# Kernel tuning notes

Hardware: AMD Instinct MI355X
Metric: run time of the kernel (lower is better)

## Reference

```python
import jax, jax.numpy as jnp
import numpy as np

GROUPS = 2
EPS = 1e-5


def channel_shuffle(x, groups=2):
    b, c, h, w = x.shape
    x = x.reshape(b, groups, c // groups, h, w)
    x = jnp.transpose(x, (0, 2, 1, 3, 4))
    return x.reshape(b, c, h, w)


def binarize_weight(w):
    # w: (O, I/g, k, k). scaling_factor = mean |w| over (in,kh,kw), detached.
    scale = jax.lax.stop_gradient(jnp.mean(jnp.abs(w), axis=(1, 2, 3), keepdims=True))
    bw = scale * jnp.sign(w)
    cl = jnp.clip(w, -1.0, 1.0)
    # STE: forward value = bw, gradient flows through clamp
    return jax.lax.stop_gradient(bw) - jax.lax.stop_gradient(cl) + cl


@jax.custom_vjp
def bin_act(x):
    return jnp.sign(x)


def _bin_act_fwd(x):
    return jnp.sign(x), x


def _bin_act_bwd(x, g):
    scale = jnp.where((x >= 1.0) | (x <= -1.0), 0.01, 1.0)
    return (g * scale,)


bin_act.defvjp(_bin_act_fwd, _bin_act_bwd)


def grouped_bin_conv(x, w, pad):
    return jax.lax.conv_general_dilated(
        x, binarize_weight(w), window_strides=(1, 1),
        padding=[(pad, pad), (pad, pad)],
        dimension_numbers=('NCHW', 'OIHW', 'NCHW'),
        feature_group_count=GROUPS)


def batchnorm(x, gamma, beta):
    # training-mode BN: biased batch statistics over (N,H,W)
    mu = jnp.mean(x, axis=(0, 2, 3), keepdims=True)
    var = jnp.mean((x - mu) ** 2, axis=(0, 2, 3), keepdims=True)
    xn = (x - mu) * jax.lax.rsqrt(var + EPS)
    return xn * gamma[None, :, None, None] + beta[None, :, None, None]


def add_bias(x, b):
    return x + b[None, :, None, None]


def prelu(x, a):
    return jnp.where(x >= 0, x, a[None, :, None, None] * x)


def setup_inputs() -> dict:
    key = jax.random.key(0)
    ks = jax.random.split(key, 4)
    C, half = 256, 128
    x = jax.random.normal(ks[0], (32, C, 56, 56), dtype=jnp.float32)
    # two BinaryConvs (64,128,3,3) stacked -> grouped (128,128,3,3)
    w3 = jax.random.uniform(ks[1], (half, C // GROUPS, 3, 3), dtype=jnp.float32) * 0.001
    w1 = jax.random.uniform(ks[2], (half, C // GROUPS, 1, 1), dtype=jnp.float32) * 0.001
    z = jnp.zeros((C,), jnp.float32)
    return {
        'x': x, 'w3': w3, 'w1': w1,
        'b1': z, 'g1': jnp.ones((half,), jnp.float32), 'be1': jnp.zeros((half,), jnp.float32),
        'b2_1': z, 'a2': jnp.full((C,), 0.25, jnp.float32), 'b2_2': z,
        'b3_1': z, 'g3': jnp.ones((half,), jnp.float32), 'be3': jnp.zeros((half,), jnp.float32),
        'b4_1': z, 'a4': jnp.full((C,), 0.25, jnp.float32), 'b4_2': z,
    }


def reference(x, w3, w1, b1, g1, be1, b2_1, a2, b2_2, b3_1, g3, be3, b4_1, a4, b4_2):
    half = w3.shape[0]  # out_channel // 2 = 128
    x = channel_shuffle(x, GROUPS)
    x1 = bin_act(add_bias(x, b1))
    x1 = batchnorm(grouped_bin_conv(x1, w3, pad=1), g1, be1)
    x1_res = x[:, half:]
    x1 = x1 + x[:, :half]
    x2 = jnp.concatenate([x1, x1_res], axis=1)
    x2 = add_bias(prelu(add_bias(x2, b2_1), a2), b2_2)
    x2 = add_bias(x2, b3_1)
    x3 = bin_act(x2)
    x3 = batchnorm(grouped_bin_conv(x3, w1, pad=0), g3, be3)
    x3_res = x2[:, half:]
    x3 = x3 + x2[:, :half]
    x4 = jnp.concatenate([x3, x3_res], axis=1)
    x5 = add_bias(prelu(add_bias(x4, b4_1), a4), b4_2)
    return x5
```

## Files before the change

### kernel.cpp

```cpp
#include <hip/hip_runtime.h>
#include <stdint.h>

typedef unsigned short ushort_t;
typedef unsigned int uint_t;
typedef _Float16 half_t;

typedef float  float4_t __attribute__((ext_vector_type(4)));
typedef float  float2_t __attribute__((ext_vector_type(2)));
typedef _Float16 half4_t __attribute__((ext_vector_type(4)));
typedef _Float16 half2_t __attribute__((ext_vector_type(2)));
typedef uint_t uint4_t  __attribute__((ext_vector_type(4)));
typedef uint_t uint2_t  __attribute__((ext_vector_type(2)));

#define B_N 32
#define C_N 256
#define HALF_N 128
#define H_N 56
#define W_N 56
#define HW_N 3136
#define NPIX (B_N * HW_N)
#define EPS_D 1e-5
#define W3S 40
#define PWS 16

__global__ void prep_kernel(const float* __restrict__ w3, const float* __restrict__ w1,
                            uint_t* __restrict__ wbits3, uint_t* __restrict__ wbits1,
                            uint_t* __restrict__ popcw3,
                            double* __restrict__ scale3, double* __restrict__ scale1,
                            double* __restrict__ sums1, double* __restrict__ sums2,
                            uint_t* __restrict__ oflags) {
    __shared__ double red[128];
    __shared__ int ipw[2][9];
    __shared__ int flsh[2];
    int t = threadIdx.x;
    int blk = blockIdx.x;
    int lane = t & 63;
    int wv = t >> 6;
    if (blk == 0) {
        sums1[t] = 0.0; sums1[128 + t] = 0.0;
        sums2[t] = 0.0; sums2[128 + t] = 0.0;
    }
    if (blk < 128) {
        int o = blk;
        double acc = 0.0;
        int anynp = 0;
        #pragma unroll
        for (int j = 0; j < 9; ++j) {
            float v = w3[o * 1152 + t * 9 + j];
            acc += fabs((double)v);
            anynp |= (v <= 0.f) ? 1 : 0;
            unsigned long long b = __ballot(v > 0.f);
            if (lane == 0) {
                wbits3[o * W3S + j * 4 + wv * 2 + 0] = (uint_t)b;
                wbits3[o * W3S + j * 4 + wv * 2 + 1] = (uint_t)(b >> 32);
                ipw[wv][j] = __popcll(b);
            }
        }
        unsigned long long m = __ballot(anynp != 0);
        if (lane == 0) flsh[wv] = (m != 0ull) ? 1 : 0;
        red[t] = acc; __syncthreads();
        for (int s = 64; s > 0; s >>= 1) { if (t < s) red[t] += red[t + s]; __syncthreads(); }
        if (t == 0) { scale3[o] = red[0] / 1152.0; oflags[o] = (uint_t)(flsh[0] | flsh[1]); }
        if (t < 9) popcw3[o * PWS + t] = (uint_t)(ipw[0][t] + ipw[1][t]);
    } else {
        int o = blk - 128;
        float v = w1[o * 128 + t];
        unsigned long long b = __ballot(v > 0.f);
        unsigned long long m = __ballot(v <= 0.f);
        if (lane == 0) {
            wbits1[o * 8 + wv * 2 + 0] = (uint_t)b;
            wbits1[o * 8 + wv * 2 + 1] = (uint_t)(b >> 32);
            flsh[wv] = (m != 0ull) ? 1 : 0;
        }
        red[t] = fabs((double)v); __syncthreads();
        for (int s = 64; s > 0; s >>= 1) { if (t < s) red[t] += red[t + s]; __syncthreads(); }
        if (t == 0) { scale1[o] = red[0] / 128.0; oflags[128 + o] = (uint_t)(flsh[0] | flsh[1]); }
    }
}

__global__ __launch_bounds__(256) void sign1_kernel(const float* __restrict__ x,
                                                    const float* __restrict__ b1,
                                                    uint_t* __restrict__ vb,
                                                    const uint_t* __restrict__ oflags,
                                                    uint_t* __restrict__ fin) {
    __shared__ int fl[4];
    int t = threadIdx.x;
    if (blockIdx.x == 0 && blockIdx.y == 0) {
        int lane = t & 63, wv4 = t >> 6;
        uint_t f = oflags[t];
        unsigned long long m = __ballot(f != 0u);
        if (lane == 0) fl[wv4] = (m != 0ull) ? 1 : 0;
        __syncthreads();
        if (t == 0) { fin[0] = (uint_t)(fl[0] | fl[1]); fin[1] = (uint_t)(fl[2] | fl[3]); }
    }
    int p = blockIdx.x * 512 + t * 2;
    int cb = blockIdx.y * 32;
    int b = p / HW_N;
    int hw = p - b * HW_N;
    const float* xb = x + (size_t)b * C_N * HW_N + hw;
    uint_t w0 = 0, w1 = 0;
    #pragma unroll
    for (int j = 0; j < 32; ++j) {
        int c = cb + j;
        int src = ((c & 1) << 7) + (c >> 1);
        float2_t xv = *(const float2_t*)(xb + (size_t)src * HW_N);
        double bc = (double)b1[c];
        if ((double)xv[0] + bc > 0.0) w0 |= (1u << j);
        if ((double)xv[1] + bc > 0.0) w1 |= (1u << j);
    }
    uint2_t o2; o2[0] = w0; o2[1] = w1;
    *(uint2_t*)(vb + (size_t)(cb >> 5) * NPIX + p) = o2;
}

__global__ __launch_bounds__(256) void conv3_kernel(const uint_t* __restrict__ vb,
                                                    const uint_t* __restrict__ wbits3,
                                                    const uint_t* __restrict__ popcw3,
                                                    half_t* __restrict__ yh,
                                                    double* __restrict__ sums,
                                                    const uint_t* __restrict__ fin) {
    __shared__ short dlds[32][258];
    __shared__ int partS[8][32];
    __shared__ int partS2[8][32];
    int t = threadIdx.x;
    int lane = t & 63;
    int wv = t >> 6;
    bool fast = (fin[0] == 0u);
    int yb = blockIdx.y;
    if (fast && (yb & 1)) return;
    int g = yb >> 1;
    int oh = yb & 1;
    int o0 = g * 64 + oh * 32;
    int p = blockIdx.x * 256 + t;
    int hw = p % HW_N;
    int h = hw / W_N;
    int w = hw - h * W_N;
    const uint_t* vbase = vb + (size_t)g * 4 * NPIX;

    uint_t v[9][4];
    int inv[9];
    int nvalid = 0;
    #pragma unroll
    for (int j = 0; j < 9; ++j) {
        int kh = j / 3 - 1, kw = j - (j / 3) * 3 - 1;
        int hh = h + kh, ww = w + kw;
        bool valid = (hh >= 0) && (hh < H_N) && (ww >= 0) && (ww < W_N);
        inv[j] = valid ? 0 : 1;
        nvalid += valid ? 1 : 0;
        int off = p + kh * W_N + kw;
        #pragma unroll
        for (int q = 0; q < 4; ++q)
            v[j][q] = valid ? vbase[(size_t)q * NPIX + off] : 0u;
    }
    int base = 128 * nvalid;

    if (fast) {
        int P = 0;
        #pragma unroll
        for (int j = 0; j < 9; ++j)
            #pragma unroll
            for (int q = 0; q < 4; ++q)
                P += __popc(v[j][q]);
        int dot = 2 * P - base;
        yh[(size_t)o0 * NPIX + p] = (half_t)(float)dot;
        int s = dot, s2 = dot * dot;
        #pragma unroll
        for (int off = 32; off > 0; off >>= 1) {
            s  += __shfl_xor(s, off);
            s2 += __shfl_xor(s2, off);
        }
        if (lane == 0) { partS[0][wv] = s; partS2[0][wv] = s2; }
        __syncthreads();
        if (t == 0) {
            partS[1][0]  = partS[0][0] + partS[0][1] + partS[0][2] + partS[0][3];
            partS2[1][0] = partS2[0][0] + partS2[0][1] + partS2[0][2] + partS2[0][3];
        }
        __syncthreads();
        if (t < 64) {
            atomicAdd(&sums[o0 + t], (double)partS[1][0]);
            atomicAdd(&sums[128 + o0 + t], (double)partS2[1][0]);
        }
        return;
    }

    half_t* yrow = yh + (size_t)o0 * NPIX + p;
    for (int oi = 0; oi < 32; ++oi) {
        const uint_t* wo = wbits3 + (size_t)(o0 + oi) * W3S;
        const uint_t* pw = popcw3 + (size_t)(o0 + oi) * PWS;
        int acc = 0;
        #pragma unroll
        for (int j = 0; j < 9; ++j)
            #pragma unroll
            for (int q = 0; q < 4; ++q)
                acc += __popc(v[j][q] ^ wo[j * 4 + q]);
        int corr = 0;
        #pragma unroll
        for (int j = 0; j < 9; ++j) corr += inv[j] * (int)pw[j];
        int dot = base - 2 * (acc - corr);
        yrow[(size_t)oi * NPIX] = (half_t)(float)dot;
        dlds[oi][t] = (short)dot;
    }
    __syncthreads();
    {
        int o = t & 31, seg = t >> 5;
        const int* r32 = (const int*)(&dlds[o][seg * 32]);
        int S = 0, S2 = 0;
        #pragma unroll
        for (int j = 0; j < 16; ++j) {
            int pr = r32[j];
            int d0 = (int)(short)(pr & 0xffff);
            int d1 = pr >> 16;
            S += d0 + d1; S2 += d0 * d0 + d1 * d1;
        }
        partS[seg][o] = S; partS2[seg][o] = S2;
    }
    __syncthreads();
    if (t < 32) {
        int S = 0, S2 = 0;
        #pragma unroll
        for (int s8 = 0; s8 < 8; ++s8) { S += partS[s8][t]; S2 += partS2[s8][t]; }
        int c = o0 + t;
        atomicAdd(&sums[c], (double)S);
        atomicAdd(&sums[128 + c], (double)S2);
    }
}

__device__ __forceinline__ void coef_entry(const double* __restrict__ sums,
                                           const double* __restrict__ scale,
                                           const float* __restrict__ gamma,
                                           const float* __restrict__ beta,
                                           int c, double* coefL) {
    double M = (double)NPIX;
    double mean = sums[c] / M;
    double var = sums[128 + c] / M - mean * mean;
    double s = scale[c];
    double r = 1.0 / sqrt(s * s * var + EPS_D);
    double g = (double)gamma[c];
    coefL[c] = s * r * g;
    coefL[128 + c] = (double)beta[c] - s * mean * r * g;
}

__device__ __forceinline__ void coef_entry_f(const double* __restrict__ sums,
                                             const double* __restrict__ scale,
                                             const float* __restrict__ gamma,
                                             const float* __restrict__ beta,
                                             int c, float* cf) {
    double M = (double)NPIX;
    double mean = sums[c] / M;
    double var = sums[128 + c] / M - mean * mean;
    double s = scale[c];
    double r = 1.0 / sqrt(s * s * var + EPS_D);
    double g = (double)gamma[c];
    cf[c] = (float)(s * r * g);
    cf[128 + c] = (float)((double)beta[c] - s * mean * r * g);
}

__device__ __forceinline__ double x2_val(double xs, double K, bool hasy,
                                         const double* coef1, int c,
                                         const float* __restrict__ b2_1, const float* __restrict__ a2,
                                         const float* __restrict__ b2_2, const float* __restrict__ b3_1) {
    int ci = c & 127;
    double t = hasy ? (coef1[ci] * K + coef1[128 + ci] + xs) : xs;
    t += (double)b2_1[c];
    double a = (double)a2[c];
    t = (t >= 0.0) ? t : a * t;
    t += (double)b2_2[c];
    t += (double)b3_1[c];
    return t;
}

__global__ __launch_bounds__(256) void x2c1_kernel(
        const float* __restrict__ x, const half_t* __restrict__ y1h,
        const double* __restrict__ sums1, const double* __restrict__ scale3,
        const float* __restrict__ g1, const float* __restrict__ be1,
        const float* __restrict__ b2_1, const float* __restrict__ a2,
        const float* __restrict__ b2_2, const float* __restrict__ b3_1,
        const uint_t* __restrict__ wbits1,
        half_t* __restrict__ y3h, double* __restrict__ sums2,
        const float* __restrict__ b4_1, const float* __restrict__ a4,
        const float* __restrict__ b4_2, float* __restrict__ out,
        const uint_t* __restrict__ fin) {
    __shared__ double coefL[256];
    __shared__ uint_t shW[128][5];
    __shared__ short dst[64][130];
    __shared__ int partS[4][64];
    __shared__ int partS2[4][64];
    int t = threadIdx.x;
    int lane = t & 63;
    int wv = t >> 6;
    int pl = t & 127;
    int ch = t >> 7;
    int g = blockIdx.y;
    bool fast3 = (fin[0] == 0u);
    bool fast1 = (fin[1] == 0u);
    if (g == 0 && t < 128) coef_entry(sums1, scale3, g1, be1, t, coefL);
    __syncthreads();

    int p = blockIdx.x * 128 + pl;
    int b = p / HW_N;
    int hw = p - b * HW_N;
    const float* xb = x + (size_t)b * C_N * HW_N + hw;

    uint_t wA = 0, wB = 0;
    if (g == 0) {
        if (fast3) {
            double K = (double)(float)y1h[(size_t)(ch * 64) * NPIX + p];
            #pragma unroll
            for (int wq = 0; wq < 2; ++wq) {
                uint_t bits = 0u;
                #pragma unroll
                for (int j = 0; j < 32; ++j) {
                    int c = ch * 64 + wq * 32 + j;
                    int src = ((c & 1) << 7) + (c >> 1);
                    double xs = (double)xb[(size_t)src * HW_N];
                    double v = x2_val(xs, K, true, coefL, c, b2_1, a2, b2_2, b3_1);
                    bits |= (v > 0.0) ? (1u << j) : 0u;
                }
                if (wq == 0) wA = bits; else wB = bits;
            }
        } else {
            #pragma unroll
            for (int wq = 0; wq < 2; ++wq) {
                uint_t bits = 0u;
                #pragma unroll
                for (int j = 0; j < 32; ++j) {
                    int c = ch * 64 + wq * 32 + j;
                    int src = ((c & 1) << 7) + (c >> 1);
                    double xs = (double)xb[(size_t)src * HW_N];
                    double K = (double)(float)y1h[(size_t)c * NPIX + p];
                    double v = x2_val(xs, K, true, coefL, c, b2_1, a2, b2_2, b3_1);
                    bits |= (v > 0.0) ? (1u << j) : 0u;
                }
                if (wq == 0) wA = bits; else wB = bits;
            }
        }
    } else {
        #pragma unroll
        for (int wq = 0; wq < 2; ++wq) {
            uint_t bits = 0u;
            #pragma unroll
            for (int j = 0; j < 32; ++j) {
                int c = 128 + ch * 64 + wq * 32 + j;
                int src = ((c & 1) << 7) + (c >> 1);
                double xs = (double)xb[(size_t)src * HW_N];
                double v = x2_val(xs, 0.0, false, coefL, c, b2_1, a2, b2_2, b3_1);
                bits |= (v > 0.0) ? (1u << j) : 0u;
                float b41c = b4_1[c], a4c = a4[c], b42c = b4_2[c];
                float f0 = (float)v + b41c;
                f0 = (f0 >= 0.f) ? f0 : a4c * f0;
                f0 += b42c;
                out[((size_t)b * C_N + c) * HW_N + hw] = f0;
            }
            if (wq == 0) wA = bits; else wB = bits;
        }
    }

    shW[pl][2 * ch + 0] = wA;
    shW[pl][2 * ch + 1] = wB;
    __syncthreads();
    uint_t W0 = shW[pl][0], W1 = shW[pl][1], W2 = shW[pl][2], W3 = shW[pl][3];

    int obase = g * 64;
    if (fast1) {
        if (ch == 0) {
            int P = __popc(W0) + __popc(W1) + __popc(W2) + __popc(W3);
            int dot = 2 * P - 128;
            y3h[(size_t)obase * NPIX + p] = (half_t)(float)dot;
            int s = dot, s2 = dot * dot;
            #pragma unroll
            for (int off = 32; off > 0; off >>= 1) {
                s  += __shfl_xor(s, off);
                s2 += __shfl_xor(s2, off);
            }
            if (lane == 0) { partS[0][wv] = s; partS2[0][wv] = s2; }
        }
        __syncthreads();
        if (t == 0) {
            partS[1][0]  = partS[0][0] + partS[0][1];
            partS2[1][0] = partS2[0][0] + partS2[0][1];
        }
        __syncthreads();
        if (t < 64) {
            atomicAdd(&sums2[obase + t], (double)partS[1][0]);
            atomicAdd(&sums2[128 + obase + t], (double)partS2[1][0]);
        }
        return;
    }

    #pragma unroll
    for (int oi = 0; oi < 32; ++oi) {
        int o = obase + ch * 32 + oi;
        const uint_t* wo = wbits1 + (size_t)o * 8;
        int acc = __popc(W0 ^ wo[0]) + __popc(W1 ^ wo[1])
                + __popc(W2 ^ wo[2]) + __popc(W3 ^ wo[3]);
        int dot = 128 - 2 * acc;
        y3h[(size_t)o * NPIX + p] = (half_t)(float)dot;
        dst[ch * 32 + oi][pl] = (short)dot;
    }
    __syncthreads();
    {
        int o = t & 63, seg = t >> 6;
        const int* r32 = (const int*)(&dst[o][seg * 32]);
        int S = 0, S2 = 0;
        #pragma unroll
        for (int j = 0; j < 16; ++j) {
            int pr = r32[j];
            int e0 = (int)(short)(pr & 0xffff);
            int e1 = pr >> 16;
            S += e0 + e1; S2 += e0 * e0 + e1 * e1;
        }
        partS[seg][o] = S; partS2[seg][o] = S2;
    }
    __syncthreads();
    if (t < 64) {
        int S  = partS[0][t] + partS[1][t] + partS[2][t] + partS[3][t];
        int S2 = partS2[0][t] + partS2[1][t] + partS2[2][t] + partS2[3][t];
        int c = obase + t;
        atomicAdd(&sums2[c], (double)S);
        atomicAdd(&sums2[128 + c], (double)S2);
    }
}

__global__ __launch_bounds__(256) void out_kernel(
        const float* __restrict__ x, const half_t* __restrict__ y1h,
        const half_t* __restrict__ y3h,
        const double* __restrict__ sums1, const double* __restrict__ scale3,
        const float* __restrict__ g1, const float* __restrict__ be1,
        const double* __restrict__ sums2, const double* __restrict__ scale1,
        const float* __restrict__ g3, const float* __restrict__ be3,
        const float* __restrict__ b2_1, const float* __restrict__ a2,
        const float* __restrict__ b2_2, const float* __restrict__ b3_1,
        const float* __restrict__ b4_1, const float* __restrict__ a4,
        const float* __restrict__ b4_2, float* __restrict__ out,
        const uint_t* __restrict__ fin) {
    __shared__ float c1f[256];
    __shared__ float c3f[256];
    int t = threadIdx.x;
    if (t < 128) coef_entry_f(sums1, scale3, g1, be1, t, c1f);
    else coef_entry_f(sums2, scale1, g3, be3, t - 128, c3f);
    __syncthreads();
    int c = blockIdx.y;
    int src = ((c & 1) << 7) + (c >> 1);
    int y1slice = (fin[0] == 0u) ? ((c < 64) ? 0 : 64) : c;
    int y3slice = (fin[1] == 0u) ? ((c < 64) ? 0 : 64) : c;
    float b21 = b2_1[c], aa2v = a2[c], b23 = b2_2[c] + b3_1[c];
    float b41 = b4_1[c], aa4v = a4[c], b42 = b4_2[c];
    float c1 = c1f[c], c1b = c1f[128 + c];
    float c3 = c3f[c], c3b = c3f[128 + c];
    const half_t* y1p = y1h + (size_t)y1slice * NPIX;
    const half_t* y3p = y3h + (size_t)y3slice * NPIX;
    #pragma unroll
    for (int i = 0; i < 2; ++i) {
        int p = blockIdx.x * 2048 + i * 1024 + t * 4;
        int b = p / HW_N;
        int hw = p - b * HW_N;
        float4_t xs = *(const float4_t*)(x + ((size_t)b * C_N + src) * HW_N + hw);
        half4_t y1v = *(const half4_t*)(y1p + p);
        half4_t y3v = *(const half4_t*)(y3p + p);
        float4_t ov;
        #pragma unroll
        for (int k = 0; k < 4; ++k) {
            float v = fmaf(c1, (float)y1v[k], c1b) + xs[k];
            v += b21;
            v = (v >= 0.f) ? v : aa2v * v;
            v += b23;
            float t2 = v;
            v = fmaf(c3, (float)y3v[k], c3b) + t2;
            v += b41;
            v = (v >= 0.f) ? v : aa4v * v;
            v += b42;
            ov[k] = v;
        }
        *(float4_t*)(out + ((size_t)b * C_N + c) * HW_N + hw) = ov;
    }
}

extern "C" void kernel_launch(void* const* d_in, const int* in_sizes, int n_in,
                              void* d_out, int out_size, void* d_ws, size_t ws_size,
                              hipStream_t stream) {
    const float* x    = (const float*)d_in[0];
    const float* w3   = (const float*)d_in[1];
    const float* w1   = (const float*)d_in[2];
    const float* b1   = (const float*)d_in[3];
    const float* g1   = (const float*)d_in[4];
    const float* be1  = (const float*)d_in[5];
    const float* b2_1 = (const float*)d_in[6];
    const float* a2   = (const float*)d_in[7];
    const float* b2_2 = (const float*)d_in[8];
    const float* b3_1 = (const float*)d_in[9];
    const float* g3   = (const float*)d_in[10];
    const float* be3  = (const float*)d_in[11];
    const float* b4_1 = (const float*)d_in[12];
    const float* a4   = (const float*)d_in[13];
    const float* b4_2 = (const float*)d_in[14];

    char* ws = (char*)d_ws;
    half_t* y1h    = (half_t*)(ws + 0);
    half_t* y3h    = (half_t*)(ws + 25690112);
    uint_t* wbits3 = (uint_t*)(ws + 51380224);
    uint_t* wbits1 = (uint_t*)(ws + 51400704);
    uint_t* popcw3 = (uint_t*)(ws + 51404800);
    double* scale3 = (double*)(ws + 51412992);
    double* scale1 = (double*)(ws + 51414016);
    double* sums1  = (double*)(ws + 51415040);
    double* sums2  = (double*)(ws + 51417088);
    uint_t* oflags = (uint_t*)(ws + 51419136);
    uint_t* fin    = (uint_t*)(ws + 51420160);

    uint_t* vb1 = (uint_t*)((char*)d_out + 0);
    float*  outp = (float*)d_out;

    prep_kernel<<<256, 128, 0, stream>>>(w3, w1, wbits3, wbits1, popcw3,
                                         scale3, scale1, sums1, sums2, oflags);
    sign1_kernel<<<dim3(NPIX / 512, 8), 256, 0, stream>>>(x, b1, vb1, oflags, fin);
    conv3_kernel<<<dim3(NPIX / 256, 4), 256, 0, stream>>>(vb1, wbits3, popcw3, y1h, sums1, fin);
    x2c1_kernel<<<dim3(NPIX / 128, 2), 256, 0, stream>>>(x, y1h, sums1, scale3, g1, be1,
                                                         b2_1, a2, b2_2, b3_1,
                                                         wbits1, y3h, sums2,
                                                         b4_1, a4, b4_2, outp, fin);
    out_kernel<<<dim3(NPIX / 2048, 128), 256, 0, stream>>>(x, y1h, y3h,
                                                           sums1, scale3, g1, be1,
                                                           sums2, scale1, g3, be3,
                                                           b2_1, a2, b2_2, b3_1,
                                                           b4_1, a4, b4_2, outp, fin);
}
```

Baseline: 314.1 us.

## Split x2c1 into a specialized fast kernel and a generic fallback kernel

Result: no change. 316.4 us (+0.7%).

```diff
diff --git a/kernel.cpp b/kernel.cpp
--- a/kernel.cpp
+++ b/kernel.cpp
@@ -268,7 +268,97 @@
     return t;
 }
 
-__global__ __launch_bounds__(256) void x2c1_kernel(
+__global__ __launch_bounds__(256, 4) void x2c1_fast_kernel(
+        const float* __restrict__ x, const half_t* __restrict__ y1h,
+        const double* __restrict__ sums1, const double* __restrict__ scale3,
+        const float* __restrict__ g1, const float* __restrict__ be1,
+        const float* __restrict__ b2_1, const float* __restrict__ a2,
+        const float* __restrict__ b2_2, const float* __restrict__ b3_1,
+        half_t* __restrict__ y3h, double* __restrict__ sums2,
+        const float* __restrict__ b4_1, const float* __restrict__ a4,
+        const float* __restrict__ b4_2, float* __restrict__ out,
+        const uint_t* __restrict__ fin) {
+    if ((fin[0] | fin[1]) != 0u) return;
+    __shared__ float tile[64][128];
+    __shared__ double coefL[256];
+    __shared__ uint_t shW[128][5];
+    __shared__ int red[4];
+    int t = threadIdx.x;
+    int lane = t & 63;
+    int w = t >> 6;
+    int g = blockIdx.y;
+    if (g == 0 && t < 128) coef_entry(sums1, scale3, g1, be1, t, coefL);
+
+    int p0 = blockIdx.x * 128;
+    int sp = p0 + 2 * lane;
+    int sb = sp / HW_N;
+    int shw = sp - sb * HW_N;
+    const float* sbase = x + (size_t)sb * C_N * HW_N + shw;
+    int pl = t & 127;
+    int h = t >> 7;
+    int p = p0 + pl;
+    int b = p / HW_N;
+    int hw = p - b * HW_N;
+    __syncthreads();
+
+    uint_t wd0 = 0, wd1 = 0;
+    #pragma unroll
+    for (int cp = 0; cp < 2; ++cp) {
+        #pragma unroll
+        for (int s = 0; s < 16; ++s) {
+            int cl = w + 4 * s;
+            int c = g * 128 + cp * 64 + cl;
+            int src = ((c & 1) << 7) + (c >> 1);
+            float2_t v = *(const float2_t*)(sbase + (size_t)src * HW_N);
+            *(float2_t*)(&tile[cl][2 * lane]) = v;
+        }
+        __syncthreads();
+        double K = 0.0;
+        if (g == 0) K = (double)(float)y1h[(size_t)(cp * 64) * NPIX + p];
+        uint_t bits = 0u;
+        #pragma unroll
+        for (int j = 0; j < 32; ++j) {
+            int cl = h * 32 + j;
+            int c = g * 128 + cp * 64 + cl;
+            double xs = (double)tile[cl][pl];
+            double v = x2_val(xs, K, g == 0, coefL, c, b2_1, a2, b2_2, b3_1);
+            bits |= (v > 0.0) ? (1u << j) : 0u;
+            if (g == 1) {
+                float b41c = b4_1[c], a4c = a4[c], b42c = b4_2[c];
+                float f0 = (float)v + b41c;
+                f0 = (f0 >= 0.f) ? f0 : a4c * f0;
+                f0 += b42c;
+                out[((size_t)b * C_N + c) * HW_N + hw] = f0;
+            }
+        }
+        shW[pl][cp * 2 + h] = bits;
+        if (cp == 0) wd0 = bits; else wd1 = bits;
+        (void)wd0; (void)wd1;
+        __syncthreads();
+    }
+
+    uint_t W0 = shW[pl][0], W1 = shW[pl][1], W2 = shW[pl][2], W3 = shW[pl][3];
+    int P = __popc(W0) + __popc(W1) + __popc(W2) + __popc(W3);
+    int dot = 2 * P - 128;
+    int obase = g * 64;
+    if (h == 0) y3h[(size_t)obase * NPIX + p] = (half_t)(float)dot;
+    int s = dot, s2 = dot * dot;
+    #pragma unroll
+    for (int off = 32; off > 0; off >>= 1) {
+        s  += __shfl_xor(s, off);
+        s2 += __shfl_xor(s2, off);
+    }
+    if (h == 0 && lane == 0) { red[w] = s; red[2 + w] = s2; }
+    __syncthreads();
+    if (t < 64) {
+        int S  = red[0] + red[1];
+        int S2 = red[2] + red[3];
+        atomicAdd(&sums2[obase + t], (double)S);
+        atomicAdd(&sums2[128 + obase + t], (double)S2);
+    }
+}
+
+__global__ __launch_bounds__(256) void x2c1_gen_kernel(
         const float* __restrict__ x, const half_t* __restrict__ y1h,
         const double* __restrict__ sums1, const double* __restrict__ scale3,
         const float* __restrict__ g1, const float* __restrict__ be1,
@@ -279,6 +369,7 @@
         const float* __restrict__ b4_1, const float* __restrict__ a4,
         const float* __restrict__ b4_2, float* __restrict__ out,
         const uint_t* __restrict__ fin) {
+    if ((fin[0] | fin[1]) == 0u) return;
     __shared__ double coefL[256];
     __shared__ uint_t shW[128][5];
     __shared__ short dst[64][130];
@@ -513,10 +604,14 @@
                                          scale3, scale1, sums1, sums2, oflags);
     sign1_kernel<<<dim3(NPIX / 512, 8), 256, 0, stream>>>(x, b1, vb1, oflags, fin);
     conv3_kernel<<<dim3(NPIX / 256, 4), 256, 0, stream>>>(vb1, wbits3, popcw3, y1h, sums1, fin);
-    x2c1_kernel<<<dim3(NPIX / 128, 2), 256, 0, stream>>>(x, y1h, sums1, scale3, g1, be1,
-                                                         b2_1, a2, b2_2, b3_1,
-                                                         wbits1, y3h, sums2,
-                                                         b4_1, a4, b4_2, outp, fin);
+    x2c1_fast_kernel<<<dim3(NPIX / 128, 2), 256, 0, stream>>>(x, y1h, sums1, scale3, g1, be1,
+                                                              b2_1, a2, b2_2, b3_1,
+                                                              y3h, sums2,
+                                                              b4_1, a4, b4_2, outp, fin);
+    x2c1_gen_kernel<<<dim3(NPIX / 128, 2), 256, 0, stream>>>(x, y1h, sums1, scale3, g1, be1,
+                                                             b2_1, a2, b2_2, b3_1,
+                                                             wbits1, y3h, sums2,
+                                                             b4_1, a4, b4_2, outp, fin);
     out_kernel<<<dim3(NPIX / 2048, 128), 256, 0, stream>>>(x, y1h, y3h,
                                                            sums1, scale3, g1, be1,
                                                            sums2, scale1, g3, be3,
```
